# Kernel tuning notes

Hardware: AMD Instinct MI355X
Metric: run time of the kernel (lower is better)

The kernel has to match this reference:

```python
import jax, jax.numpy as jnp
from jax import lax
import numpy as np

H = W = 768
N_BOXES = 512
C1, C2 = 32, 64
POOL = 5
NUM_CLASSES = 4
BN_EPS = 1e-5


def setup_inputs() -> dict:
    key = jax.random.key(0)
    ks = jax.random.split(key, 20)
    image = jax.random.normal(ks[0], (1, 3, H, W), jnp.float32)
    # valid boxes: xmax>xmin, ymax>ymin, inside [0, W)
    xmin = jax.random.randint(ks[1], (N_BOXES,), 0, W - 256)
    ymin = jax.random.randint(ks[2], (N_BOXES,), 0, H - 256)
    bw = jax.random.randint(ks[3], (N_BOXES,), 8, 256)
    bh = jax.random.randint(ks[4], (N_BOXES,), 8, 256)
    boxes = jnp.stack([xmin, ymin, xmin + bw, ymin + bh], axis=1).astype(jnp.int32)
    conv1_w = jax.random.normal(ks[5], (C1, 3, 3, 3), jnp.float32) * 0.1
    conv1_b = jax.random.normal(ks[6], (C1,), jnp.float32) * 0.01
    bn1_g = 1.0 + 0.1 * jax.random.normal(ks[7], (C1,), jnp.float32)
    bn1_b = 0.1 * jax.random.normal(ks[8], (C1,), jnp.float32)
    bn1_m = 0.1 * jax.random.normal(ks[9], (C1,), jnp.float32)
    bn1_v = jax.random.uniform(ks[10], (C1,), jnp.float32, 0.5, 1.5)
    conv2_w = jax.random.normal(ks[11], (C2, C1, 3, 3), jnp.float32) * 0.05
    conv2_b = jax.random.normal(ks[12], (C2,), jnp.float32) * 0.01
    bn2_g = 1.0 + 0.1 * jax.random.normal(ks[13], (C2,), jnp.float32)
    bn2_b = 0.1 * jax.random.normal(ks[14], (C2,), jnp.float32)
    bn2_m = 0.1 * jax.random.normal(ks[15], (C2,), jnp.float32)
    bn2_v = jax.random.uniform(ks[16], (C2,), jnp.float32, 0.5, 1.5)
    fc1_w = jax.random.normal(ks[17], (128, C2 * POOL * POOL), jnp.float32) * 0.02
    fc1_b = jnp.zeros((128,), jnp.float32)
    fc2_w = jax.random.normal(ks[18], (NUM_CLASSES, 128), jnp.float32) * 0.05
    fc2_b = jnp.zeros((NUM_CLASSES,), jnp.float32)
    return dict(image=image, boxes=boxes,
                conv1_w=conv1_w, conv1_b=conv1_b, bn1_g=bn1_g, bn1_b=bn1_b, bn1_m=bn1_m, bn1_v=bn1_v,
                conv2_w=conv2_w, conv2_b=conv2_b, bn2_g=bn2_g, bn2_b=bn2_b, bn2_m=bn2_m, bn2_v=bn2_v,
                fc1_w=fc1_w, fc1_b=fc1_b, fc2_w=fc2_w, fc2_b=fc2_b)


def _conv(x, w, b):
    y = lax.conv_general_dilated(x, w, (1, 1), ((1, 1), (1, 1)),
                                 dimension_numbers=("NCHW", "OIHW", "NCHW"))
    return y + b[None, :, None, None]


def _bn(x, g, b, m, v):
    scale = g / jnp.sqrt(v + BN_EPS)
    return x * scale[None, :, None, None] + (b - m * scale)[None, :, None, None]


def _forward(image, boxes, conv1_w, conv1_b, bn1_g, bn1_b, bn1_m, bn1_v,
             conv2_w, conv2_b, bn2_g, bn2_b, bn2_m, bn2_v,
             fc1_w, fc1_b, fc2_w, fc2_b):
    # backbone: Conv -> ReLU -> BN (order as in source), twice
    x = _bn(jax.nn.relu(_conv(image, conv1_w, conv1_b)), bn1_g, bn1_b, bn1_m, bn1_v)
    x = _bn(jax.nn.relu(_conv(x, conv2_w, conv2_b)), bn2_g, bn2_b, bn2_m, bn2_v)
    feat = x[0]  # [C2, H, W], batch assumed 1 as in the per-box slicing loop
    # integral image for exact adaptive-avg-pool over integer index rectangles
    integ = jnp.pad(feat, ((0, 0), (1, 0), (1, 0))).cumsum(1).cumsum(2)  # [C2,H+1,W+1]
    xmin, ymin, xmax, ymax = boxes[:, 0], boxes[:, 1], boxes[:, 2], boxes[:, 3]
    bh = ymax - ymin
    bw = xmax - xmin
    i = jnp.arange(POOL)
    # AdaptiveAvgPool2d bin edges: start=floor(i*L/5), end=ceil((i+1)*L/5)
    y0 = ymin[:, None] + (i * bh[:, None]) // POOL            # [N,5]
    y1 = ymin[:, None] + ((i + 1) * bh[:, None] + POOL - 1) // POOL
    x0 = xmin[:, None] + (i * bw[:, None]) // POOL
    x1 = xmin[:, None] + ((i + 1) * bw[:, None] + POOL - 1) // POOL

    def rect(ys, xs):  # [C2, N, 5, 5]
        return integ[:, ys[:, :, None], xs[:, None, :]]

    s = rect(y1, x1) - rect(y0, x1) - rect(y1, x0) + rect(y0, x0)
    area = ((y1 - y0)[:, :, None] * (x1 - x0)[:, None, :]).astype(feat.dtype)  # [N,5,5]
    pooled = s / area[None]                                    # [C2,N,5,5]
    flat = pooled.transpose(1, 0, 2, 3).reshape(boxes.shape[0], -1)  # [N, C2*25]
    h1 = jax.nn.relu(flat @ fc1_w.T + fc1_b)  # dropout is identity in eval
    return h1 @ fc2_w.T + fc2_b               # [N, num_classes]


def reference(image, boxes, conv1_w, conv1_b, bn1_g, bn1_b, bn1_m, bn1_v,
              conv2_w, conv2_b, bn2_g, bn2_b, bn2_m, bn2_v,
              fc1_w, fc1_b, fc2_w, fc2_b):
    return _forward(image, boxes, conv1_w, conv1_b, bn1_g, bn1_b, bn1_m, bn1_v,
                    conv2_w, conv2_b, bn2_g, bn2_b, bn2_m, bn2_v,
                    fc1_w, fc1_b, fc2_w, fc2_b)
```

## Files before the change

kernel.cpp:

```cpp
#include <hip/hip_runtime.h>
#include <hip/hip_bf16.h>

#define HH 768
#define WW 768
#define HWSZ (HH*WW)
#define BN_EPS 1e-5f
#define SEG 8
#define NSEG 96

typedef __attribute__((ext_vector_type(8))) short bf16x8;
typedef __attribute__((ext_vector_type(4))) float f32x4;

__device__ __forceinline__ float bf2f(unsigned short u) {
  union { unsigned int i; float f; } v; v.i = ((unsigned int)u) << 16; return v.f;
}
__device__ __forceinline__ unsigned short f2bf(float f) {
  union { float f; unsigned int i; } v; v.f = f;
  unsigned int x = v.i;
  return (unsigned short)((x + 0x7fffu + ((x >> 16) & 1u)) >> 16);
}
__device__ __forceinline__ float ldf(const void* p, int i, int flag) {
  return flag ? bf2f(((const unsigned short*)p)[i]) : ((const float*)p)[i];
}

#define DPP_ADD(v, CTRL) do {                                              \
    union { float f; int i; } _u; _u.f = (v);                              \
    int _t = __builtin_amdgcn_update_dpp(0, _u.i, (CTRL), 0xf, 0xf, true); \
    union { int i; float f; } _w; _w.i = _t;                               \
    (v) += _w.f;                                                           \
  } while (0)
__device__ __forceinline__ float row_prefix16(float v) {
  DPP_ADD(v, 0x111);
  DPP_ADD(v, 0x112);
  DPP_ADD(v, 0x114);
  DPP_ADD(v, 0x118);
  return v;
}

__device__ __forceinline__ int detect_flag(const void* v1) {
  const unsigned short* v1raw = (const unsigned short*)v1;
  int ok = 1;
  #pragma unroll
  for (int j = 0; j < 4; ++j) {
    unsigned short u = v1raw[2*j];
    if (u < 0x3E00u || u > 0x4040u) ok = 0;
  }
  return ok;
}

__global__ void k_prep(const void* __restrict__ c1b,
                       const void* __restrict__ g1, const void* __restrict__ b1,
                       const void* __restrict__ m1, const void* __restrict__ v1,
                       const void* __restrict__ c2b, const void* __restrict__ g2,
                       const void* __restrict__ b2, const void* __restrict__ m2,
                       const void* __restrict__ v2, const void* __restrict__ w1,
                       const void* __restrict__ fb1, const void* __restrict__ fw2,
                       const void* __restrict__ fb2, const void* __restrict__ w2,
                       const void* __restrict__ fw1,
                       int* __restrict__ flagp, float* __restrict__ cst,
                       unsigned short* __restrict__ A2, unsigned short* __restrict__ A1,
                       unsigned short* __restrict__ w1c)
{
  int flag = detect_flag(v1);
  int tid = threadIdx.x, bid = blockIdx.x;
  int gid = bid * 256 + tid;

  if (bid == 0) {
    if (tid == 0) *flagp = flag;
    float* bias1 = cst + 864;
    float* sc1   = cst + 896;
    float* sh1   = cst + 928;
    float* bias2 = cst + 960;
    float* sc2   = cst + 1024;
    float* sh2   = cst + 1088;
    float* fb1c  = cst + 1152;
    float* w2c   = cst + 1280;
    float* fb2c  = cst + 1792;
    if (tid < 32) {
      float s = ldf(g1, tid, flag) * rsqrtf(ldf(v1, tid, flag) + BN_EPS);
      sc1[tid] = s;
      sh1[tid] = ldf(b1, tid, flag) - ldf(m1, tid, flag) * s;
      bias1[tid] = ldf(c1b, tid, flag);
    }
    if (tid < 64) {
      float s = ldf(g2, tid, flag) * rsqrtf(ldf(v2, tid, flag) + BN_EPS);
      sc2[tid] = s;
      sh2[tid] = ldf(b2, tid, flag) - ldf(m2, tid, flag) * s;
      bias2[tid] = ldf(c2b, tid, flag);
    }
    if (tid < 128) fb1c[tid] = ldf(fb1, tid, flag);
    if (tid < 4)   fb2c[tid] = ldf(fb2, tid, flag);
    for (int i = tid; i < 512; i += 256) w2c[i] = ldf(fw2, i, flag);
  }
  if (gid < 80*288) {
    int o = gid / 288, k = gid % 288, tap = k >> 5, ci = k & 31;
    A2[gid] = (o < 64) ? f2bf(ldf(w2, (o*32 + ci)*9 + tap, flag)) : (unsigned short)0;
  }
  if (gid < 32*64) {
    int o = gid >> 6, k = gid & 63, tap = k >> 2, ci = k & 3;
    A1[gid] = (tap < 9 && ci < 3) ? f2bf(ldf(w1, o*27 + ci*9 + tap, flag))
                                  : (unsigned short)0;
  }
  for (int i = gid; i < 128*1600; i += 128*256) {
    int t = i / 1600, r = i % 1600, cell = r >> 6, c = r & 63;
    w1c[i] = f2bf(ldf(fw1, t*1600 + c*25 + cell, flag));
  }
}

__global__ __launch_bounds__(256) void k_conv1m(const void* __restrict__ img,
    const int* __restrict__ flagp, const unsigned short* __restrict__ A1,
    const float* __restrict__ cst, unsigned short* __restrict__ feat1)
{
  const float* bias1 = cst + 864;
  const float* sc1   = cst + 896;
  const float* sh1   = cst + 928;
  int flag = *flagp;
  __shared__ unsigned short tile[18 * 34 * 4];
  int tid = threadIdx.x;
  int x0 = blockIdx.x * 32, ybase = blockIdx.y * 16;

  for (int idx = tid; idx < 18*34; idx += 256) {
    int r = idx / 34, p = idx % 34;
    int gy = ybase - 1 + r, gx = x0 - 1 + p;
    unsigned short e0 = 0, e1 = 0, e2 = 0;
    if (gy >= 0 && gy < HH && gx >= 0 && gx < WW) {
      e0 = f2bf(ldf(img, 0*HWSZ + gy*WW + gx, flag));
      e1 = f2bf(ldf(img, 1*HWSZ + gy*WW + gx, flag));
      e2 = f2bf(ldf(img, 2*HWSZ + gy*WW + gx, flag));
    }
    ushort4 pk; pk.x = e0; pk.y = e1; pk.z = e2; pk.w = 0;
    *(ushort4*)(tile + idx*4) = pk;
  }

  int w = tid >> 6, lane = tid & 63, quad = lane >> 4, l16 = lane & 15;
  bf16x8 a1f[2][2];
  #pragma unroll
  for (int mt = 0; mt < 2; ++mt)
    #pragma unroll
    for (int kt = 0; kt < 2; ++kt)
      a1f[mt][kt] = *(const bf16x8*)(A1 + (mt*16 + l16)*64 + kt*32 + quad*8);
  int t0 = 2*quad, t1 = 2*quad + 1;
  int ky0 = t0/3, kx0 = t0%3, ky1 = t1/3, kx1 = t1%3;
  __syncthreads();

  for (int dyw = 0; dyw < 4; ++dyw) {
    int dy = dyw*4 + w;
    int y = ybase + dy;
    f32x4 acc[2][2];
    #pragma unroll
    for (int mt = 0; mt < 2; ++mt)
      #pragma unroll
      for (int i = 0; i < 2; ++i)
        acc[mt][i] = (f32x4){0.f,0.f,0.f,0.f};
    #pragma unroll
    for (int i = 0; i < 2; ++i) {
      int pxb = i*16 + l16;
      union { uint2 u[2]; bf16x8 v; } b0;
      b0.u[0] = *(const uint2*)(tile + ((dy + ky0)*34 + pxb + kx0)*4);
      b0.u[1] = *(const uint2*)(tile + ((dy + ky1)*34 + pxb + kx1)*4);
      union { uint2 u[2]; bf16x8 v; } b1v;
      b1v.u[0] = *(const uint2*)(tile + ((dy + 2)*34 + pxb + 2)*4);
      b1v.u[1] = make_uint2(0u, 0u);
      #pragma unroll
      for (int mt = 0; mt < 2; ++mt) {
        acc[mt][i] = __builtin_amdgcn_mfma_f32_16x16x32_bf16(a1f[mt][0], b0.v, acc[mt][i], 0, 0, 0);
        acc[mt][i] = __builtin_amdgcn_mfma_f32_16x16x32_bf16(a1f[mt][1], b1v.v, acc[mt][i], 0, 0, 0);
      }
    }
    #pragma unroll
    for (int mt = 0; mt < 2; ++mt) {
      int cb = mt*16 + quad*4;
      float bs0 = bias1[cb], bs1 = bias1[cb+1], bs2 = bias1[cb+2], bs3 = bias1[cb+3];
      float s0 = sc1[cb], s1 = sc1[cb+1], s2 = sc1[cb+2], s3 = sc1[cb+3];
      float h0 = sh1[cb], h1 = sh1[cb+1], h2 = sh1[cb+2], h3 = sh1[cb+3];
      #pragma unroll
      for (int i = 0; i < 2; ++i) {
        int px = x0 + i*16 + l16;
        ushort4 pk;
        pk.x = f2bf(fmaxf(acc[mt][i][0] + bs0, 0.f) * s0 + h0);
        pk.y = f2bf(fmaxf(acc[mt][i][1] + bs1, 0.f) * s1 + h1);
        pk.z = f2bf(fmaxf(acc[mt][i][2] + bs2, 0.f) * s2 + h2);
        pk.w = f2bf(fmaxf(acc[mt][i][3] + bs3, 0.f) * s3 + h3);
        *(ushort4*)(feat1 + ((size_t)(y*WW + px))*32 + cb) = pk;
      }
    }
  }
}

__global__ __launch_bounds__(256) void k_conv2t(const unsigned short* __restrict__ feat1,
    const unsigned short* __restrict__ A2, const float* __restrict__ cst,
    float* __restrict__ T)
{
  const float* bias2 = cst + 960;
  const float* sc2   = cst + 1024;
  const float* sh2   = cst + 1088;
  __shared__ unsigned short tile[10 * 34 * 40];
  int tid = threadIdx.x;
  int xb = blockIdx.x, ys = blockIdx.y;
  int x0 = xb * 32, ybase = ys * SEG;

  for (int idx = tid; idx < 10*34*4; idx += 256) {
    int q = idx & 3, p = (idx >> 2) % 34, r = idx / 136;
    int gy = ybase - 1 + r, gx = x0 - 1 + p;
    uint4 val = make_uint4(0u, 0u, 0u, 0u);
    if (gy >= 0 && gy < HH && gx >= 0 && gx < WW)
      val = *(const uint4*)(feat1 + (gy*WW + gx)*32 + q*8);
    *(uint4*)(tile + (r*34 + p)*40 + q*8) = val;
  }

  int w = tid >> 6, lane = tid & 63, quad = lane >> 4, l16 = lane & 15;
  int m = w * 16 + l16;
  bf16x8 afrag[9];
  #pragma unroll
  for (int t = 0; t < 9; ++t)
    afrag[t] = *(const bf16x8*)(A2 + m*288 + t*32 + quad*8);
  float bs[4], scv[4], shv[4];
  #pragma unroll
  for (int r = 0; r < 4; ++r) {
    int c = w*16 + quad*4 + r;
    bs[r] = bias2[c]; scv[r] = sc2[c]; shv[r] = sh2[c];
  }
  __syncthreads();

  f32x4 ys0 = (f32x4){0.f,0.f,0.f,0.f};
  f32x4 ys1 = (f32x4){0.f,0.f,0.f,0.f};
  int cbase = w*16 + quad*4;
  for (int dy = 0; dy < SEG; ++dy) {
    int y = ybase + dy;
    f32x4 acc[2];
    acc[0] = (f32x4){0.f,0.f,0.f,0.f};
    acc[1] = (f32x4){0.f,0.f,0.f,0.f};
    #pragma unroll
    for (int t = 0; t < 9; ++t) {
      int ky = t / 3, kx = t % 3;
      #pragma unroll
      for (int i = 0; i < 2; ++i) {
        int px = i*16 + l16 + kx;
        bf16x8 b = *(const bf16x8*)(tile + ((dy + ky)*34 + px)*40 + quad*8);
        acc[i] = __builtin_amdgcn_mfma_f32_16x16x32_bf16(afrag[t], b, acc[i], 0, 0, 0);
      }
    }
    #pragma unroll
    for (int r = 0; r < 4; ++r) {
      float v0 = fmaxf(acc[0][r] + bs[r], 0.f) * scv[r] + shv[r];
      float v1 = fmaxf(acc[1][r] + bs[r], 0.f) * scv[r] + shv[r];
      v0 = row_prefix16(v0);
      v1 = row_prefix16(v1);
      v1 += __shfl(v0, 15, 16);
      ys0[r] += v0;
      ys1[r] += v1;
    }
    *(f32x4*)(T + ((size_t)(y*WW + x0 + l16))*64 + cbase)      = ys0;
    *(f32x4*)(T + ((size_t)(y*WW + x0 + 16 + l16))*64 + cbase) = ys1;
  }
}

__global__ __launch_bounds__(256) void k_cgen_i(const float* __restrict__ T,
                                                float* __restrict__ C)
{
  int j = blockIdx.x;
  int c = threadIdx.x & 63, g = threadIdx.x >> 6;
  __shared__ float gtot[4][64];
  float run = 0.f;
  #pragma unroll 4
  for (int ii = 0; ii < 24; ++ii) {
    int i = g*24 + ii;
    run += T[((size_t)((i*SEG + SEG-1)*WW + j*32 + 31))*64 + c];
    C[((size_t)(i*24 + j))*64 + c] = run;
  }
  gtot[g][c] = run;
  __syncthreads();
  if (g > 0) {
    float off = 0.f;
    for (int gg = 0; gg < g; ++gg) off += gtot[gg][c];
    for (int ii = 0; ii < 24; ++ii) {
      int i = g*24 + ii;
      C[((size_t)(i*24 + j))*64 + c] += off;
    }
  }
}
__global__ __launch_bounds__(64) void k_cgen_j(float* __restrict__ C)
{
  int i = blockIdx.x, c = threadIdx.x;
  float run = 0.f;
  #pragma unroll
  for (int j = 0; j < 24; ++j) {
    size_t idx = ((size_t)(i*24 + j))*64 + c;
    run += C[idx];
    C[idx] = run;
  }
}

__global__ __launch_bounds__(256) void k_ab(const float* __restrict__ T,
    const float* __restrict__ C, float* __restrict__ A, float* __restrict__ Bp)
{
  int part = blockIdx.y, tid = threadIdx.x;
  int c = tid & 63, s = tid >> 6;
  if (part == 0) {
    int y = blockIdx.x * 4 + s;
    float run = 0.f;
    #pragma unroll
    for (int j = 0; j < 24; ++j) {
      run += T[((size_t)(y*WW + j*32 + 31))*64 + c];
      A[((size_t)(y*24 + j))*64 + c] = run;
    }
  } else {
    int x = blockIdx.x * 4 + s;
    int j = x >> 5;
    float run = 0.f;
    #pragma unroll 4
    for (int i = 0; i < NSEG; ++i) {
      run += T[((size_t)((i*SEG + SEG-1)*WW + x))*64 + c];
      float cj = (j > 0) ? C[((size_t)(i*24 + (j-1)))*64 + c] : 0.f;
      Bp[((size_t)(i*WW + x))*64 + c] = run + cj;
    }
  }
}

__device__ __forceinline__ float icorner(const float* __restrict__ T,
    const float* __restrict__ A, const float* __restrict__ Bp,
    int c, int yy, int xx)
{
  int i = yy >> 3, j = xx >> 5;
  float v = T[((size_t)(yy*WW + xx))*64 + c];
  if (j > 0) v += A[((size_t)(yy*24 + (j-1)))*64 + c];
  if (i > 0) v += Bp[((size_t)((i-1)*WW + xx))*64 + c];
  return v;
}

__global__ __launch_bounds__(256) void k_roi3(const float* __restrict__ T,
    const float* __restrict__ A, const float* __restrict__ Bp,
    const int* __restrict__ boxes, unsigned short* __restrict__ flat)
{
  int b = blockIdx.x;
  int xmin = boxes[b*4 + 0], ymin = boxes[b*4 + 1];
  int xmax = boxes[b*4 + 2], ymax = boxes[b*4 + 3];
  int bh = ymax - ymin, bw = xmax - xmin;
  for (int idx = threadIdx.x; idx < 1600; idx += 256) {
    int c = idx & 63, cell = idx >> 6, i = cell / 5, j = cell % 5;
    int y0 = ymin + (i*bh)/5,  y1 = ymin + ((i+1)*bh + 4)/5;
    int x0 = xmin + (j*bw)/5,  x1 = xmin + ((j+1)*bw + 4)/5;
    float s = icorner(T, A, Bp, c, y1-1, x1-1);
    if (y0 > 0)           s -= icorner(T, A, Bp, c, y0-1, x1-1);
    if (x0 > 0)           s -= icorner(T, A, Bp, c, y1-1, x0-1);
    if (y0 > 0 && x0 > 0) s += icorner(T, A, Bp, c, y0-1, x0-1);
    float area = (float)((y1 - y0) * (x1 - x0));
    flat[b*1600 + cell*64 + c] = f2bf(s / area);
  }
}

__global__ __launch_bounds__(256) void k_fcm(const unsigned short* __restrict__ flat,
    const unsigned short* __restrict__ w1c, const float* __restrict__ cst,
    const int* __restrict__ flagp, void* __restrict__ out)
{
  const float* fb1c = cst + 1152;
  const float* w2c  = cst + 1280;
  const float* fb2c = cst + 1792;
  __shared__ unsigned short sflat[16 * 1608];
  __shared__ float hbuf[16 * 132];
  int tid = threadIdx.x;
  int b0 = blockIdx.x * 16;
  for (int ii = tid; ii < 3200; ii += 256) {
    int bi = ii / 200, ch = ii % 200;
    *(uint4*)(sflat + bi*1608 + ch*8) = *(const uint4*)(flat + (b0 + bi)*1600 + ch*8);
  }
  __syncthreads();
  int w = tid >> 6, lane = tid & 63, quad = lane >> 4, l16 = lane & 15;
  f32x4 acc[2];
  acc[0] = (f32x4){0.f,0.f,0.f,0.f};
  acc[1] = (f32x4){0.f,0.f,0.f,0.f};
  for (int kt = 0; kt < 50; ++kt) {
    bf16x8 b = *(const bf16x8*)(sflat + l16*1608 + kt*32 + quad*8);
    #pragma unroll
    for (int mt = 0; mt < 2; ++mt) {
      bf16x8 a = *(const bf16x8*)(w1c + ((w*2 + mt)*16 + l16)*1600 + kt*32 + quad*8);
      acc[mt] = __builtin_amdgcn_mfma_f32_16x16x32_bf16(a, b, acc[mt], 0, 0, 0);
    }
  }
  #pragma unroll
  for (int mt = 0; mt < 2; ++mt) {
    #pragma unroll
    for (int r = 0; r < 4; ++r) {
      int h = (w*2 + mt)*16 + quad*4 + r;
      hbuf[l16*132 + h] = fmaxf(acc[mt][r] + fb1c[h], 0.f);
    }
  }
  __syncthreads();
  if (tid < 64) {
    int bi = tid >> 2, o = tid & 3;
    float a2 = fb2c[o];
    for (int k = 0; k < 128; ++k) a2 += hbuf[bi*132 + k] * w2c[o*128 + k];
    if (*flagp) ((unsigned short*)out)[(b0 + bi)*4 + o] = f2bf(a2);
    else        ((float*)out)[(b0 + bi)*4 + o] = a2;
  }
}

__global__ __launch_bounds__(256) void k_conv2_c16(const unsigned short* __restrict__ feat1,
    const unsigned short* __restrict__ A2, const float* __restrict__ cst,
    float* __restrict__ chunk, int c0, int cnw)
{
  const float* bias2 = cst + 960;
  const float* sc2   = cst + 1024;
  const float* sh2   = cst + 1088;
  __shared__ unsigned short tile[3 * 130 * 40];
  int tid = threadIdx.x;
  int y = blockIdx.y, x0 = blockIdx.x * 128;
  for (int idx = tid; idx < 3*130*4; idx += 256) {
    int q = idx & 3, p = (idx >> 2) % 130, r = idx / 520;
    int gy = y - 1 + r, gx = x0 - 1 + p;
    uint4 val = make_uint4(0u, 0u, 0u, 0u);
    if (gy >= 0 && gy < HH && gx >= 0 && gx < WW)
      val = *(const uint4*)(feat1 + (gy*WW + gx)*32 + q*8);
    *(uint4*)(tile + (r*130 + p)*40 + q*8) = val;
  }
  __syncthreads();
  int w = tid >> 6, lane = tid & 63, quad = lane >> 4, l16 = lane & 15;
  int m = c0 + l16;
  f32x4 acc[2];
  acc[0] = (f32x4){0.f,0.f,0.f,0.f};
  acc[1] = (f32x4){0.f,0.f,0.f,0.f};
  #pragma unroll
  for (int t = 0; t < 9; ++t) {
    int ky = t / 3, kx = t % 3;
    bf16x8 a = *(const bf16x8*)(A2 + m*288 + t*32 + quad*8);
    #pragma unroll
    for (int i = 0; i < 2; ++i) {
      int px = w*32 + i*16 + l16 + kx;
      bf16x8 b = *(const bf16x8*)(tile + (ky*130 + px)*40 + quad*8);
      acc[i] = __builtin_amdgcn_mfma_f32_16x16x32_bf16(a, b, acc[i], 0, 0, 0);
    }
  }
  #pragma unroll
  for (int r = 0; r < 4; ++r) {
    int cl = quad*4 + r;
    if (cl < cnw) {
      int c = c0 + cl;
      float bsv = bias2[c], s = sc2[c], sh = sh2[c];
      float* dst = chunk + cl*HWSZ + y*WW;
      #pragma unroll
      for (int i = 0; i < 2; ++i) {
        float v = fmaxf(acc[i][r] + bsv, 0.f) * s + sh;
        dst[x0 + w*32 + i*16 + l16] = v;
      }
    }
  }
}
__global__ __launch_bounds__(256) void k_csy(float* __restrict__ buf) {
  int t = blockIdx.x * 256 + threadIdx.x;
  int c = t / WW, x = t % WW;
  float* p = buf + c*HWSZ + x;
  float run = 0.f;
  for (int yb = 0; yb < HH; yb += 16) {
    float v[16];
    #pragma unroll
    for (int j = 0; j < 16; ++j) v[j] = p[(yb + j) * WW];
    #pragma unroll
    for (int j = 0; j < 16; ++j) { run += v[j]; v[j] = run; }
    #pragma unroll
    for (int j = 0; j < 16; ++j) p[(yb + j) * WW] = v[j];
  }
}
__global__ __launch_bounds__(256) void k_csx(float* __restrict__ buf) {
  int row = blockIdx.x * 4 + (threadIdx.x >> 6);
  int lane = threadIdx.x & 63;
  float* p = buf + (long)row * WW;
  float carry = 0.f;
  for (int ch = 0; ch < 12; ++ch) {
    float v = p[ch*64 + lane];
    #pragma unroll
    for (int off = 1; off < 64; off <<= 1) {
      float t = __shfl_up(v, off);
      v = (lane >= off) ? v + t : v;
    }
    v += carry;
    p[ch*64 + lane] = v;
    carry = __shfl(v, 63);
  }
}
__global__ __launch_bounds__(256) void k_roi(const float* __restrict__ integ,
    const int* __restrict__ boxes, unsigned short* __restrict__ flat, int c0, int cn)
{
  int b = blockIdx.x;
  int xmin = boxes[b*4 + 0], ymin = boxes[b*4 + 1];
  int xmax = boxes[b*4 + 2], ymax = boxes[b*4 + 3];
  int bh = ymax - ymin, bw = xmax - xmin;
  for (int idx = threadIdx.x; idx < cn*25; idx += 256) {
    int cl = idx / 25, cell = idx % 25, i = cell / 5, j = cell % 5;
    int y0 = ymin + (i*bh)/5,      y1 = ymin + ((i+1)*bh + 4)/5;
    int x0 = xmin + (j*bw)/5,      x1 = xmin + ((j+1)*bw + 4)/5;
    const float* I = integ + cl*HWSZ;
    float a  = I[(y1-1)*WW + (x1-1)];
    float bl = (y0 > 0) ? I[(y0-1)*WW + (x1-1)] : 0.f;
    float cr = (x0 > 0) ? I[(y1-1)*WW + (x0-1)] : 0.f;
    float d  = (y0 > 0 && x0 > 0) ? I[(y0-1)*WW + (x0-1)] : 0.f;
    float s = a - bl - cr + d;
    float area = (float)((y1 - y0) * (x1 - x0));
    flat[b*1600 + cell*64 + (c0 + cl)] = f2bf(s / area);
  }
}

extern "C" void kernel_launch(void* const* d_in, const int* in_sizes, int n_in,
                              void* d_out, int out_size, void* d_ws, size_t ws_size,
                              hipStream_t stream) {
  const void* img = d_in[0];
  const int* boxes = (const int*)d_in[1];
  const void* c1w = d_in[2];  const void* c1b = d_in[3];
  const void* g1  = d_in[4];  const void* b1  = d_in[5];
  const void* m1  = d_in[6];  const void* v1  = d_in[7];
  const void* c2w = d_in[8];  const void* c2b = d_in[9];
  const void* g2  = d_in[10]; const void* b2  = d_in[11];
  const void* m2  = d_in[12]; const void* v2  = d_in[13];
  const void* fw1 = d_in[14]; const void* fb1 = d_in[15];
  const void* fw2 = d_in[16]; const void* fb2 = d_in[17];

  char* ws = (char*)d_ws;
  unsigned short* A2 = (unsigned short*)ws;
  unsigned short* A1 = (unsigned short*)(ws + 46080);
  float* cst = (float*)(ws + 50176);
  int* flag = (int*)(ws + 57360);
  unsigned short* w1c  = (unsigned short*)(ws + 3592224);
  unsigned short* flat = (unsigned short*)(ws + 4001824);
  unsigned short* feat1 = (unsigned short*)(ws + 7278624);
  float* T = (float*)(ws + 45027360);
  float* Aarr = (float*)(ws + 7278624);
  float* Bparr = Aarr + (size_t)768*24*64;
  float* Carr = Bparr + (size_t)NSEG*768*64;

  const size_t base = 45027360;
  int cn;
  if      (ws_size >= base + 64ull*HWSZ*4) cn = 64;
  else if (ws_size >= base + 16ull*HWSZ*4) cn = 16;
  else if (ws_size >= base +  8ull*HWSZ*4) cn = 8;
  else if (ws_size >= base +  4ull*HWSZ*4) cn = 4;
  else if (ws_size >= base +  2ull*HWSZ*4) cn = 2;
  else                                     cn = 1;

  hipLaunchKernelGGL(k_prep, dim3(128), dim3(256), 0, stream,
                     c1b, g1, b1, m1, v1, c2b, g2, b2, m2, v2, c1w,
                     fb1, fw2, fb2, c2w, fw1, flag, cst, A2, A1, w1c);
  hipLaunchKernelGGL(k_conv1m, dim3(24, 48), dim3(256), 0, stream,
                     img, flag, A1, cst, feat1);

  if (cn == 64) {
    hipLaunchKernelGGL(k_conv2t, dim3(24, NSEG), dim3(256), 0, stream,
                       feat1, A2, cst, T);
    hipLaunchKernelGGL(k_cgen_i, dim3(24), dim3(256), 0, stream, T, Carr);
    hipLaunchKernelGGL(k_cgen_j, dim3(NSEG), dim3(64), 0, stream, Carr);
    hipLaunchKernelGGL(k_ab, dim3(192, 2), dim3(256), 0, stream, T, Carr, Aarr, Bparr);
    hipLaunchKernelGGL(k_roi3, dim3(512), dim3(256), 0, stream,
                       T, Aarr, Bparr, boxes, flat);
  } else {
    for (int c0 = 0; c0 < 64; c0 += cn) {
      hipLaunchKernelGGL(k_conv2_c16, dim3(6, 768), dim3(256), 0, stream,
                         feat1, A2, cst, T, c0, cn);
      hipLaunchKernelGGL(k_csy, dim3(cn*3), dim3(256), 0, stream, T);
      hipLaunchKernelGGL(k_csx, dim3(cn*192), dim3(256), 0, stream, T);
      hipLaunchKernelGGL(k_roi, dim3(512), dim3(256), 0, stream, T, boxes, flat, c0, cn);
    }
  }
  hipLaunchKernelGGL(k_fcm, dim3(32), dim3(256), 0, stream, flat, w1c, cst, flag,
                     d_out);
}
```

Baseline: 225.3 us.

## Merge post-conv prefix-sum and ROI kernels into one cooperative kernel

```diff
diff --git a/kernel.cpp b/kernel.cpp
--- a/kernel.cpp
+++ b/kernel.cpp
@@ -1,5 +1,8 @@
 #include <hip/hip_runtime.h>
 #include <hip/hip_bf16.h>
+#include <hip/hip_cooperative_groups.h>
+
+namespace cg = cooperative_groups;
 
 #define HH 768
 #define WW 768
@@ -250,62 +253,64 @@
       ys0[r] += v0;
       ys1[r] += v1;
     }
-    *(f32x4*)(T + ((size_t)(y*WW + x0 + l16))*64 + cbase)      = ys0;
-    *(f32x4*)(T + ((size_t)(y*WW + x0 + 16 + l16))*64 + cbase) = ys1;
-  }
-}
-
-__global__ __launch_bounds__(256) void k_cgen_i(const float* __restrict__ T,
-                                                float* __restrict__ C)
-{
-  int j = blockIdx.x;
-  int c = threadIdx.x & 63, g = threadIdx.x >> 6;
-  __shared__ float gtot[4][64];
-  float run = 0.f;
-  #pragma unroll 4
-  for (int ii = 0; ii < 24; ++ii) {
-    int i = g*24 + ii;
-    run += T[((size_t)((i*SEG + SEG-1)*WW + j*32 + 31))*64 + c];
-    C[((size_t)(i*24 + j))*64 + c] = run;
-  }
-  gtot[g][c] = run;
-  __syncthreads();
-  if (g > 0) {
-    float off = 0.f;
-    for (int gg = 0; gg < g; ++gg) off += gtot[gg][c];
-    for (int ii = 0; ii < 24; ++ii) {
-      int i = g*24 + ii;
-      C[((size_t)(i*24 + j))*64 + c] += off;
-    }
-  }
-}
-__global__ __launch_bounds__(64) void k_cgen_j(float* __restrict__ C)
-{
-  int i = blockIdx.x, c = threadIdx.x;
-  float run = 0.f;
-  #pragma unroll
-  for (int j = 0; j < 24; ++j) {
-    size_t idx = ((size_t)(i*24 + j))*64 + c;
-    run += C[idx];
-    C[idx] = run;
-  }
-}
-
-__global__ __launch_bounds__(256) void k_ab(const float* __restrict__ T,
-    const float* __restrict__ C, float* __restrict__ A, float* __restrict__ Bp)
-{
-  int part = blockIdx.y, tid = threadIdx.x;
+    __builtin_nontemporal_store(ys0, (f32x4*)(T + ((size_t)(y*WW + x0 + l16))*64 + cbase));
+    __builtin_nontemporal_store(ys1, (f32x4*)(T + ((size_t)(y*WW + x0 + 16 + l16))*64 + cbase));
+  }
+}
+
+__device__ __forceinline__ float icorner(const float* __restrict__ T,
+    const float* __restrict__ A, const float* __restrict__ Bp,
+    int c, int yy, int xx)
+{
+  int i = yy >> 3, j = xx >> 5;
+  float v = T[((size_t)(yy*WW + xx))*64 + c];
+  if (j > 0) v += A[((size_t)(yy*24 + (j-1)))*64 + c];
+  if (i > 0) v += Bp[((size_t)((i-1)*WW + xx))*64 + c];
+  return v;
+}
+
+__global__ __launch_bounds__(256) void k_post(const float* __restrict__ T,
+    float* __restrict__ C, float* __restrict__ A, float* __restrict__ Bp,
+    const int* __restrict__ boxes, unsigned short* __restrict__ flat)
+{
+  cg::grid_group grid = cg::this_grid();
+  __shared__ float Sp[NSEG*24];
+  int bid = blockIdx.x, tid = threadIdx.x;
   int c = tid & 63, s = tid >> 6;
-  if (part == 0) {
-    int y = blockIdx.x * 4 + s;
+
+  if (bid < 192) {
+    int y = bid * 4 + s;
     float run = 0.f;
     #pragma unroll
     for (int j = 0; j < 24; ++j) {
       run += T[((size_t)(y*WW + j*32 + 31))*64 + c];
       A[((size_t)(y*24 + j))*64 + c] = run;
     }
-  } else {
-    int x = blockIdx.x * 4 + s;
+  } else if (bid < 256) {
+    int cc = bid - 192;
+    for (int idx = tid; idx < NSEG*24; idx += 256) {
+      int i = idx / 24, j = idx % 24;
+      Sp[idx] = T[((size_t)((i*SEG + SEG-1)*WW + j*32 + 31))*64 + cc];
+    }
+    __syncthreads();
+    if (tid < 24) {
+      float run = 0.f;
+      for (int i = 0; i < NSEG; ++i) { run += Sp[i*24 + tid]; Sp[i*24 + tid] = run; }
+    }
+    __syncthreads();
+    if (tid < NSEG) {
+      float run = 0.f;
+      #pragma unroll
+      for (int j = 0; j < 24; ++j) { run += Sp[tid*24 + j]; Sp[tid*24 + j] = run; }
+    }
+    __syncthreads();
+    for (int idx = tid; idx < NSEG*24; idx += 256)
+      C[((size_t)idx)*64 + cc] = Sp[idx];
+  }
+  grid.sync();
+
+  if (bid < 192) {
+    int x = bid * 4 + s;
     int j = x >> 5;
     float run = 0.f;
     #pragma unroll 4
@@ -315,37 +320,22 @@
       Bp[((size_t)(i*WW + x))*64 + c] = run + cj;
     }
   }
-}
-
-__device__ __forceinline__ float icorner(const float* __restrict__ T,
-    const float* __restrict__ A, const float* __restrict__ Bp,
-    int c, int yy, int xx)
-{
-  int i = yy >> 3, j = xx >> 5;
-  float v = T[((size_t)(yy*WW + xx))*64 + c];
-  if (j > 0) v += A[((size_t)(yy*24 + (j-1)))*64 + c];
-  if (i > 0) v += Bp[((size_t)((i-1)*WW + xx))*64 + c];
-  return v;
-}
-
-__global__ __launch_bounds__(256) void k_roi3(const float* __restrict__ T,
-    const float* __restrict__ A, const float* __restrict__ Bp,
-    const int* __restrict__ boxes, unsigned short* __restrict__ flat)
-{
-  int b = blockIdx.x;
+  grid.sync();
+
+  int b = bid;
   int xmin = boxes[b*4 + 0], ymin = boxes[b*4 + 1];
   int xmax = boxes[b*4 + 2], ymax = boxes[b*4 + 3];
   int bh = ymax - ymin, bw = xmax - xmin;
-  for (int idx = threadIdx.x; idx < 1600; idx += 256) {
-    int c = idx & 63, cell = idx >> 6, i = cell / 5, j = cell % 5;
+  for (int idx = tid; idx < 1600; idx += 256) {
+    int cc = idx & 63, cell = idx >> 6, i = cell / 5, j = cell % 5;
     int y0 = ymin + (i*bh)/5,  y1 = ymin + ((i+1)*bh + 4)/5;
     int x0 = xmin + (j*bw)/5,  x1 = xmin + ((j+1)*bw + 4)/5;
-    float s = icorner(T, A, Bp, c, y1-1, x1-1);
-    if (y0 > 0)           s -= icorner(T, A, Bp, c, y0-1, x1-1);
-    if (x0 > 0)           s -= icorner(T, A, Bp, c, y1-1, x0-1);
-    if (y0 > 0 && x0 > 0) s += icorner(T, A, Bp, c, y0-1, x0-1);
+    float sv = icorner(T, A, Bp, cc, y1-1, x1-1);
+    if (y0 > 0)           sv -= icorner(T, A, Bp, cc, y0-1, x1-1);
+    if (x0 > 0)           sv -= icorner(T, A, Bp, cc, y1-1, x0-1);
+    if (y0 > 0 && x0 > 0) sv += icorner(T, A, Bp, cc, y0-1, x0-1);
     float area = (float)((y1 - y0) * (x1 - x0));
-    flat[b*1600 + cell*64 + c] = f2bf(s / area);
+    flat[b*1600 + cell*64 + cc] = f2bf(sv / area);
   }
 }
 
@@ -544,11 +534,10 @@
   if (cn == 64) {
     hipLaunchKernelGGL(k_conv2t, dim3(24, NSEG), dim3(256), 0, stream,
                        feat1, A2, cst, T);
-    hipLaunchKernelGGL(k_cgen_i, dim3(24), dim3(256), 0, stream, T, Carr);
-    hipLaunchKernelGGL(k_cgen_j, dim3(NSEG), dim3(64), 0, stream, Carr);
-    hipLaunchKernelGGL(k_ab, dim3(192, 2), dim3(256), 0, stream, T, Carr, Aarr, Bparr);
-    hipLaunchKernelGGL(k_roi3, dim3(512), dim3(256), 0, stream,
-                       T, Aarr, Bparr, boxes, flat);
+    const float* Tc = T;
+    void* args[] = { (void*)&Tc, (void*)&Carr, (void*)&Aarr, (void*)&Bparr,
+                     (void*)&boxes, (void*)&flat };
+    hipLaunchCooperativeKernel((void*)k_post, dim3(512), dim3(256), args, 0, stream);
   } else {
     for (int c0 = 0; c0 < 64; c0 += cn) {
       hipLaunchKernelGGL(k_conv2_c16, dim3(6, 768), dim3(256), 0, stream,
```

After: 471.7 us. +109.4%, slower.
